# Kernel optimization log

Measured on AMD Instinct MI355X. Metric: run time of the kernel, lower is better.

Reference implementation:

```python
import jax, jax.numpy as jnp
import numpy as np

B, T, D, V, MEM = 2, 512, 512, 256, 256


def _gru(x, h0, wih, whh, bih, bhh):
    # x: [B,T,D], h0: [B,D]; torch GRU gate order: r, z, n
    def step(h, xt):
        gi = xt @ wih.T + bih            # [B,3D]
        gh = h @ whh.T + bhh             # [B,3D]
        i_r, i_z, i_n = jnp.split(gi, 3, axis=-1)
        h_r, h_z, h_n = jnp.split(gh, 3, axis=-1)
        r = jax.nn.sigmoid(i_r + h_r)
        z = jax.nn.sigmoid(i_z + h_z)
        n = jnp.tanh(i_n + r * h_n)
        h_new = (1.0 - z) * n + z * h
        return h_new, h_new
    hT, ys = jax.lax.scan(step, h0, jnp.swapaxes(x, 0, 1))
    return jnp.swapaxes(ys, 0, 1), hT


def _layernorm(x, g, b, eps=1e-5):
    m = jnp.mean(x, axis=-1, keepdims=True)
    v = jnp.mean((x - m) ** 2, axis=-1, keepdims=True)
    return (x - m) / jnp.sqrt(v + eps) * g + b


def setup_inputs() -> dict:
    key = jax.random.key(0)
    ks = jax.random.split(key, 24)
    s = 1.0 / np.sqrt(D)
    inp = {
        'x': jax.random.randint(ks[0], (B, T), 0, V, dtype=jnp.int32),
        'h_f': jnp.zeros((1, B, D), jnp.float32),
        'h_s': jnp.zeros((1, B, D), jnp.float32),
        'soma_w': jax.random.normal(ks[1], (V, D), jnp.float32),
        'fast_wih': jax.random.normal(ks[2], (3 * D, D)) * s,
        'fast_whh': jax.random.normal(ks[3], (3 * D, D)) * s,
        'fast_bih': jax.random.normal(ks[4], (3 * D,)) * s,
        'fast_bhh': jax.random.normal(ks[5], (3 * D,)) * s,
        'slow_wih': jax.random.normal(ks[6], (3 * D, D)) * s,
        'slow_whh': jax.random.normal(ks[7], (3 * D, D)) * s,
        'slow_bih': jax.random.normal(ks[8], (3 * D,)) * s,
        'slow_bhh': jax.random.normal(ks[9], (3 * D,)) * s,
        'qkv_w': jax.random.normal(ks[10], (3 * D, D)) * s,
        'qkv_b': jax.random.normal(ks[11], (3 * D,)) * s,
        'gate_w': jax.random.normal(ks[12], (D, D)) * s,
        'gate_b': jax.random.normal(ks[13], (D,)) * s,
        'gate_g': jnp.ones((D,), jnp.float32),
        'gate_bb': jnp.zeros((D,), jnp.float32),
        'mem_bank': jax.random.normal(ks[14], (MEM, D)) * 0.1,
        'hip_qw': jax.random.normal(ks[15], (D, D)) * s,
        'hip_qb': jax.random.normal(ks[16], (D,)) * s,
        'axon_w': jax.random.normal(ks[17], (D, 4 * D)) * (0.5 * s),
        'axon_b': jax.random.normal(ks[18], (D,)) * s,
        'norm_g': jnp.ones((D,), jnp.float32),
        'norm_b': jnp.zeros((D,), jnp.float32),
    }
    return inp


def reference(x, h_f, h_s, soma_w, fast_wih, fast_whh, fast_bih, fast_bhh,
              slow_wih, slow_whh, slow_bih, slow_bhh, qkv_w, qkv_b,
              gate_w, gate_b, gate_g, gate_bb, mem_bank, hip_qw, hip_qb,
              axon_w, axon_b, norm_g, norm_b):
    d = soma_w.shape[1]
    s_in = soma_w[x]  # mod[0] == 1.0
    p_f, hf1 = _gru(s_in, h_f[0], fast_wih, fast_whh, fast_bih, fast_bhh)
    p_s, hs1 = _gru(p_f, h_s[0], slow_wih, slow_whh, slow_bih, slow_bhh)
    # LinearIntentMemory: naive cumulative outer-product linear attention
    qkv = p_s @ qkv_w.T + qkv_b
    q, k, v = jnp.split(qkv, 3, axis=-1)
    q = jax.nn.elu(q) + 1.0
    k = jax.nn.elu(k) + 1.0
    kv_cum = jnp.cumsum(jnp.einsum('bti,btj->btij', k, v), axis=1)  # [B,T,D,D]
    num = jnp.einsum('bti,btij->btj', q, kv_cum)
    den = jnp.einsum('bti,bti->bt', q, jnp.cumsum(k, axis=1))[..., None] + 1e-6
    l_mem = num / den
    # intent gate: Linear -> LayerNorm -> Tanh
    intent = jnp.tanh(_layernorm(p_s @ gate_w.T + gate_b, gate_g, gate_bb))
    # hippocampus: softmax attention over memory bank
    qh = p_s @ hip_qw.T + hip_qb
    attn = qh @ mem_bank.T / jnp.sqrt(jnp.float32(d))
    episodes = jax.nn.softmax(attn, axis=-1) @ mem_bank
    combined = jnp.concatenate([p_f, intent, l_mem, episodes], axis=-1)
    thought = _layernorm(jnp.tanh(combined @ axon_w.T + axon_b), norm_g, norm_b)
    sw = soma_w / jnp.maximum(jnp.linalg.norm(soma_w, axis=-1, keepdims=True), 1e-12)
    logits = (thought @ sw.T) * 16.0
    return (logits, thought, hf1[None], hs1[None])
```

## Files before the change

### kernel.cpp

```cpp
#include <hip/hip_runtime.h>
#include <cstddef>

#define F_ELUQK 1
#define F_CAUSAL 2
#define F_DIV 4
#define F_NN 8
#define F_SCALE 16
#define FLAG_STRIDE 32
#define L_WGS 64
#define UNITS 8

enum : int {
  OFF_QH = 0,
  OFF_GI = 524288,
  OFF_COMB = OFF_GI + 1572864,
  OFF_PS = OFF_COMB + 2097152,
  OFF_QKV = OFF_PS + 524288,
  OFF_SCORES = OFF_QKV + 1572864,
  OFF_DEN = OFF_SCORES + 524288,
  OFF_TMP = OFF_DEN + 1024,
  OFF_ATTN = OFF_TMP + 524288,
  OFF_SW = OFF_ATTN + 262144,
  OFF_RING = OFF_SW + 131072,
  OFF_HSB = OFF_RING + 4096,
  OFF_FLAGS = OFF_HSB + 2048
};

__global__ __launch_bounds__(256) void gemm(
    const float* __restrict__ A, int lda, const float* __restrict__ B, int ldb,
    float* __restrict__ C, int ldc, int coff, int K,
    const float* __restrict__ bias, const float* __restrict__ den,
    float scale, int flags, int bBatch, const int* __restrict__ xidx) {
  __shared__ float As[16 * 65];
  __shared__ float Bs[16 * 65];
  int tid = threadIdx.x;
  int n0 = blockIdx.x * 64, m0 = blockIdx.y * 64;
  int rowoff = (m0 >> 9) * bBatch;
  int tx = tid & 15, ty = tid >> 4;

  if ((flags & F_CAUSAL) && n0 > ((m0 & 511) + 63)) {
    #pragma unroll
    for (int i = 0; i < 4; ++i)
      #pragma unroll
      for (int j = 0; j < 4; ++j)
        C[(size_t)(m0 + ty * 4 + i) * ldc + coff + n0 + tx * 4 + j] = 0.f;
    return;
  }

  float acc[4][4] = {};
  for (int k0 = 0; k0 < K; k0 += 16) {
    {
      int rr = tid >> 2, c4 = (tid & 3) << 2;
      int arow = m0 + rr;
      const float* ap = xidx ? (A + (size_t)xidx[arow] * 512 + (k0 + c4))
                             : (A + (size_t)arow * lda + (k0 + c4));
      float4 av = *(const float4*)ap;
      As[(c4 + 0) * 65 + rr] = av.x;
      As[(c4 + 1) * 65 + rr] = av.y;
      As[(c4 + 2) * 65 + rr] = av.z;
      As[(c4 + 3) * 65 + rr] = av.w;
    }
    if (!(flags & F_NN)) {
      int rr = tid >> 2, c4 = (tid & 3) << 2;
      const float* bp = B + (size_t)(n0 + rr + rowoff) * ldb + (k0 + c4);
      float4 bv = *(const float4*)bp;
      Bs[(c4 + 0) * 65 + rr] = bv.x; Bs[(c4 + 1) * 65 + rr] = bv.y;
      Bs[(c4 + 2) * 65 + rr] = bv.z; Bs[(c4 + 3) * 65 + rr] = bv.w;
    } else {
      int kk = tid >> 4, n4 = (tid & 15) << 2;
      const float* bp = B + (size_t)(k0 + kk + rowoff) * ldb + (n0 + n4);
      float4 bv = *(const float4*)bp;
      Bs[kk * 65 + n4 + 0] = bv.x; Bs[kk * 65 + n4 + 1] = bv.y;
      Bs[kk * 65 + n4 + 2] = bv.z; Bs[kk * 65 + n4 + 3] = bv.w;
    }
    __syncthreads();
    #pragma unroll
    for (int k = 0; k < 16; ++k) {
      float av[4], bv[4];
      #pragma unroll
      for (int i = 0; i < 4; ++i) av[i] = As[k * 65 + ty * 4 + i];
      #pragma unroll
      for (int j = 0; j < 4; ++j) bv[j] = Bs[k * 65 + tx * 4 + j];
      #pragma unroll
      for (int i = 0; i < 4; ++i)
        #pragma unroll
        for (int j = 0; j < 4; ++j)
          acc[i][j] = fmaf(av[i], bv[j], acc[i][j]);
    }
    __syncthreads();
  }
  #pragma unroll
  for (int i = 0; i < 4; ++i) {
    int m = m0 + ty * 4 + i;
    float dv = (flags & F_DIV) ? (1.0f / (den[m] + 1e-6f)) : 1.0f;
    #pragma unroll
    for (int j = 0; j < 4; ++j) {
      int n = n0 + tx * 4 + j;
      float v = acc[i][j];
      if (bias) v += bias[n];
      if (flags & F_ELUQK) { if (n < 1024) v = (v > 0.f) ? (v + 1.f) : __expf(v); }
      if (flags & F_CAUSAL) { if (n > (m & 511)) v = 0.f; }
      if (flags & F_SCALE) v *= scale;
      if (flags & F_DIV) v *= dv;
      C[(size_t)m * ldc + coff + n] = v;
    }
  }
}

__global__ __launch_bounds__(256) void gemm3(
    const float* __restrict__ A,
    const float* __restrict__ qkvw, const float* __restrict__ qkvb,
    const float* __restrict__ gatew, const float* __restrict__ gateb,
    const float* __restrict__ hipw, const float* __restrict__ hipb,
    float* __restrict__ QKV, float* __restrict__ TMP, float* __restrict__ QH) {
  __shared__ float As[16 * 65];
  __shared__ float Bs[16 * 65];
  int tid = threadIdx.x;
  int n0 = blockIdx.x * 64, m0 = blockIdx.y * 64;
  const float* B; const float* bias; float* C; int ldc, base;
  if (n0 < 1536) { B = qkvw; bias = qkvb; C = QKV; ldc = 1536; base = 0; }
  else if (n0 < 2048) { B = gatew; bias = gateb; C = TMP; ldc = 512; base = 1536; }
  else { B = hipw; bias = hipb; C = QH; ldc = 512; base = 2048; }
  int tx = tid & 15, ty = tid >> 4;
  float acc[4][4] = {};
  for (int k0 = 0; k0 < 512; k0 += 16) {
    {
      int rr = tid >> 2, c4 = (tid & 3) << 2;
      const float* ap = A + (size_t)(m0 + rr) * 512 + (k0 + c4);
      float4 av = *(const float4*)ap;
      As[(c4 + 0) * 65 + rr] = av.x; As[(c4 + 1) * 65 + rr] = av.y;
      As[(c4 + 2) * 65 + rr] = av.z; As[(c4 + 3) * 65 + rr] = av.w;
    }
    {
      int rr = tid >> 2, c4 = (tid & 3) << 2;
      const float* bp = B + (size_t)(n0 - base + rr) * 512 + (k0 + c4);
      float4 bv = *(const float4*)bp;
      Bs[(c4 + 0) * 65 + rr] = bv.x; Bs[(c4 + 1) * 65 + rr] = bv.y;
      Bs[(c4 + 2) * 65 + rr] = bv.z; Bs[(c4 + 3) * 65 + rr] = bv.w;
    }
    __syncthreads();
    #pragma unroll
    for (int k = 0; k < 16; ++k) {
      float av[4], bv[4];
      #pragma unroll
      for (int i = 0; i < 4; ++i) av[i] = As[k * 65 + ty * 4 + i];
      #pragma unroll
      for (int j = 0; j < 4; ++j) bv[j] = Bs[k * 65 + tx * 4 + j];
      #pragma unroll
      for (int i = 0; i < 4; ++i)
        #pragma unroll
        for (int j = 0; j < 4; ++j)
          acc[i][j] = fmaf(av[i], bv[j], acc[i][j]);
    }
    __syncthreads();
  }
  #pragma unroll
  for (int i = 0; i < 4; ++i) {
    int m = m0 + ty * 4 + i;
    #pragma unroll
    for (int j = 0; j < 4; ++j) {
      int n = n0 + tx * 4 + j;
      float v = acc[i][j] + bias[n - base];
      if (n < 1024) v = (v > 0.f) ? (v + 1.f) : __expf(v);
      C[(size_t)m * ldc + (n - base)] = v;
    }
  }
}

__device__ __forceinline__ void post_flag(unsigned* flags, int w, unsigned v) {
  __hip_atomic_store(flags + (size_t)w * FLAG_STRIDE, v, __ATOMIC_RELAXED,
                     __HIP_MEMORY_SCOPE_AGENT);
}
__device__ __forceinline__ void poll64(const unsigned* flags, unsigned tgt, int lane) {
  const unsigned* p = flags + (size_t)lane * FLAG_STRIDE;
  while (__hip_atomic_load(p, __ATOMIC_RELAXED, __HIP_MEMORY_SCOPE_AGENT) < tgt)
    __builtin_amdgcn_s_sleep(1);
}

__global__ __launch_bounds__(256, 1) void gru2_kernel(
    const float* __restrict__ gi,
    const float* __restrict__ fwhh, const float* __restrict__ fbhh,
    const float* __restrict__ h0f,
    const float* __restrict__ swih, const float* __restrict__ sbih,
    const float* __restrict__ swhh, const float* __restrict__ sbhh,
    const float* __restrict__ h0s,
    float* __restrict__ pf_out,
    float* __restrict__ ps_out,
    float* __restrict__ hfT, float* __restrict__ hsT,
    float* __restrict__ ring,
    float* __restrict__ hsbuf,
    unsigned* __restrict__ flagsA, unsigned* __restrict__ flagsB) {
  __shared__ __attribute__((aligned(16))) float hl[1024];
  __shared__ __attribute__((aligned(16))) float hfs[1024];
  __shared__ float P[48];
  __shared__ float Q[48];
  __shared__ float bl[24];
  __shared__ float bi[24];
  int tid = threadIdx.x, wg = blockIdx.x;
  bool L1 = wg < L_WGS;
  int j0 = (wg & (L_WGS - 1)) * UNITS;
  int part = tid & 7, r = tid >> 3;
  int g = r >> 3, u = r & 7;
  int wave = tid >> 6, lane = tid & 63;
  const float* whh = L1 ? fwhh : swhh;
  const float* bhh = L1 ? fbhh : sbhh;

  float4 wh[16], wi[16];
  if (r < 24) {
    const float* wp = whh + (size_t)(g * 512 + j0 + u) * 512 + part * 4;
    #pragma unroll
    for (int i = 0; i < 16; ++i) wh[i] = *(const float4*)(wp + i * 32);
    if (!L1) {
      const float* wp2 = swih + (size_t)(g * 512 + j0 + u) * 512 + part * 4;
      #pragma unroll
      for (int i = 0; i < 16; ++i) wi[i] = *(const float4*)(wp2 + i * 32);
    }
  }
  if (tid < 24) {
    bl[tid] = bhh[(tid >> 3) * 512 + j0 + (tid & 7)];
    if (!L1) bi[tid] = sbih[(tid >> 3) * 512 + j0 + (tid & 7)];
  }

  unsigned long long* hlq = (unsigned long long*)hl;
  unsigned long long* hfq = (unsigned long long*)hfs;
  const float4* h4 = (const float4*)hl;
  const float4* f4v = (const float4*)hfs;

  if (L1) {
    for (int t = 0; t < 512; ++t) {
      float i_r = 0.f, i_z = 0.f, i_n = 0.f;
      if (tid < 16) {
        int b = tid >> 3, jl = tid & 7;
        const float* girow = gi + (size_t)(b * 512 + t) * 1536 + j0 + jl;
        i_r = girow[0]; i_z = girow[512]; i_n = girow[1024];
      }
      if (wave == 0) {
        if (t > 0) poll64(flagsA, (unsigned)t, lane);
        unsigned long long v[8];
        if (t == 0) {
          const unsigned long long* s8 = (const unsigned long long*)h0f;
          #pragma unroll
          for (int k = 0; k < 8; ++k) v[k] = s8[k * 64 + lane];
        } else {
          const unsigned long long* s8 =
              (const unsigned long long*)(ring + ((t - 1) & 3) * 1024);
          #pragma unroll
          for (int k = 0; k < 8; ++k)
            v[k] = __hip_atomic_load(s8 + k * 64 + lane, __ATOMIC_RELAXED,
                                     __HIP_MEMORY_SCOPE_AGENT);
        }
        #pragma unroll
        for (int k = 0; k < 8; ++k) hlq[k * 64 + lane] = v[k];
      } else if (wave == 1) {
        if (t >= 4) poll64(flagsB, (unsigned)(t - 3), lane);
      }
      __syncthreads();
      if (r < 24) {
        float a0 = 0.f, a1 = 0.f;
        #pragma unroll
        for (int i = 0; i < 16; ++i) {
          float4 w = wh[i];
          float4 x0 = h4[i * 8 + part];
          float4 x1 = h4[128 + i * 8 + part];
          a0 += w.x * x0.x + w.y * x0.y + w.z * x0.z + w.w * x0.w;
          a1 += w.x * x1.x + w.y * x1.y + w.z * x1.z + w.w * x1.w;
        }
        a0 += __shfl_xor(a0, 1); a0 += __shfl_xor(a0, 2); a0 += __shfl_xor(a0, 4);
        a1 += __shfl_xor(a1, 1); a1 += __shfl_xor(a1, 2); a1 += __shfl_xor(a1, 4);
        if (part == 0) { P[r] = a0; P[24 + r] = a1; }
      }
      __syncthreads();
      if (tid < 16) {
        int b = tid >> 3, u2 = tid & 7, j = j0 + u2;
        float gh_r = P[b * 24 + u2] + bl[u2];
        float gh_z = P[b * 24 + 8 + u2] + bl[8 + u2];
        float gh_n = P[b * 24 + 16 + u2] + bl[16 + u2];
        float hold = hl[b * 512 + j];
        float rg = 1.0f / (1.0f + __expf(-(i_r + gh_r)));
        float zg = 1.0f / (1.0f + __expf(-(i_z + gh_z)));
        float ng = tanhf(i_n + rg * gh_n);
        float hnew = (1.0f - zg) * ng + zg * hold;
        __hip_atomic_store(ring + (size_t)(t & 3) * 1024 + b * 512 + j, hnew,
                           __ATOMIC_RELAXED, __HIP_MEMORY_SCOPE_AGENT);
        pf_out[(size_t)(b * 512 + t) * 2048 + j] = hnew;
        if (t == 511) hfT[b * 512 + j] = hnew;
      }
      __syncthreads();
      if (tid == 0) post_flag(flagsA, wg, (unsigned)(t + 1));
    }
  } else {
    for (int t2 = 0; t2 < 512; ++t2) {
      if (wave == 0) {
        poll64(flagsA, (unsigned)(t2 + 1), lane);
        const unsigned long long* f8 =
            (const unsigned long long*)(ring + (t2 & 3) * 1024);
        unsigned long long v[8];
        #pragma unroll
        for (int k = 0; k < 8; ++k)
          v[k] = __hip_atomic_load(f8 + k * 64 + lane, __ATOMIC_RELAXED,
                                   __HIP_MEMORY_SCOPE_AGENT);
        #pragma unroll
        for (int k = 0; k < 8; ++k) hfq[k * 64 + lane] = v[k];
      } else if (wave == 1) {
        unsigned long long v[8];
        if (t2 == 0) {
          const unsigned long long* s8 = (const unsigned long long*)h0s;
          #pragma unroll
          for (int k = 0; k < 8; ++k) v[k] = s8[k * 64 + lane];
        } else {
          poll64(flagsB, (unsigned)t2, lane);
          const unsigned long long* s8 =
              (const unsigned long long*)(hsbuf + ((t2 - 1) & 1) * 1024);
          #pragma unroll
          for (int k = 0; k < 8; ++k)
            v[k] = __hip_atomic_load(s8 + k * 64 + lane, __ATOMIC_RELAXED,
                                     __HIP_MEMORY_SCOPE_AGENT);
        }
        #pragma unroll
        for (int k = 0; k < 8; ++k) hlq[k * 64 + lane] = v[k];
      }
      __syncthreads();
      if (r < 24) {
        float a0 = 0.f, a1 = 0.f, c0 = 0.f, c1 = 0.f;
        #pragma unroll
        for (int i = 0; i < 16; ++i) {
          float4 w = wh[i];
          float4 x0 = h4[i * 8 + part];
          float4 x1 = h4[128 + i * 8 + part];
          a0 += w.x * x0.x + w.y * x0.y + w.z * x0.z + w.w * x0.w;
          a1 += w.x * x1.x + w.y * x1.y + w.z * x1.z + w.w * x1.w;
          float4 v = wi[i];
          float4 y0 = f4v[i * 8 + part];
          float4 y1 = f4v[128 + i * 8 + part];
          c0 += v.x * y0.x + v.y * y0.y + v.z * y0.z + v.w * y0.w;
          c1 += v.x * y1.x + v.y * y1.y + v.z * y1.z + v.w * y1.w;
        }
        a0 += __shfl_xor(a0, 1); a0 += __shfl_xor(a0, 2); a0 += __shfl_xor(a0, 4);
        a1 += __shfl_xor(a1, 1); a1 += __shfl_xor(a1, 2); a1 += __shfl_xor(a1, 4);
        c0 += __shfl_xor(c0, 1); c0 += __shfl_xor(c0, 2); c0 += __shfl_xor(c0, 4);
        c1 += __shfl_xor(c1, 1); c1 += __shfl_xor(c1, 2); c1 += __shfl_xor(c1, 4);
        if (part == 0) { P[r] = a0; P[24 + r] = a1; Q[r] = c0; Q[24 + r] = c1; }
      }
      __syncthreads();
      if (tid < 16) {
        int b = tid >> 3, u2 = tid & 7, j = j0 + u2;
        float i_r = Q[b * 24 + u2] + bi[u2];
        float i_z = Q[b * 24 + 8 + u2] + bi[8 + u2];
        float i_n = Q[b * 24 + 16 + u2] + bi[16 + u2];
        float gh_r = P[b * 24 + u2] + bl[u2];
        float gh_z = P[b * 24 + 8 + u2] + bl[8 + u2];
        float gh_n = P[b * 24 + 16 + u2] + bl[16 + u2];
        float hold = hl[b * 512 + j];
        float rg = 1.0f / (1.0f + __expf(-(i_r + gh_r)));
        float zg = 1.0f / (1.0f + __expf(-(i_z + gh_z)));
        float ng = tanhf(i_n + rg * gh_n);
        float hnew = (1.0f - zg) * ng + zg * hold;
        __hip_atomic_store(hsbuf + (size_t)(t2 & 1) * 1024 + b * 512 + j, hnew,
                           __ATOMIC_RELAXED, __HIP_MEMORY_SCOPE_AGENT);
        ps_out[(size_t)(b * 512 + t2) * 512 + j] = hnew;
        if (t2 == 511) hsT[b * 512 + j] = hnew;
      }
      __syncthreads();
      if (tid == 0) post_flag(flagsB, wg - L_WGS, (unsigned)(t2 + 1));
    }
  }
}

__global__ __launch_bounds__(256) void rowsum_kernel(const float* __restrict__ S,
                                                     float* __restrict__ den) {
  int m = blockIdx.x, tid = threadIdx.x;
  float s = S[(size_t)m * 512 + tid] + S[(size_t)m * 512 + 256 + tid];
  #pragma unroll
  for (int off = 32; off > 0; off >>= 1) s += __shfl_down(s, off);
  __shared__ float r4[4];
  if ((tid & 63) == 0) r4[tid >> 6] = s;
  __syncthreads();
  if (tid == 0) den[m] = r4[0] + r4[1] + r4[2] + r4[3];
}

__global__ __launch_bounds__(256) void softmax_kernel(float* __restrict__ a) {
  int m = blockIdx.x, tid = threadIdx.x;
  float v = a[(size_t)m * 256 + tid];
  float mx = v;
  #pragma unroll
  for (int off = 32; off > 0; off >>= 1) mx = fmaxf(mx, __shfl_down(mx, off));
  __shared__ float r4[4];
  __shared__ float s4[4];
  if ((tid & 63) == 0) r4[tid >> 6] = mx;
  __syncthreads();
  mx = fmaxf(fmaxf(r4[0], r4[1]), fmaxf(r4[2], r4[3]));
  float e = __expf(v - mx);
  float s = e;
  #pragma unroll
  for (int off = 32; off > 0; off >>= 1) s += __shfl_down(s, off);
  if ((tid & 63) == 0) s4[tid >> 6] = s;
  __syncthreads();
  s = s4[0] + s4[1] + s4[2] + s4[3];
  a[(size_t)m * 256 + tid] = e / s;
}

__global__ __launch_bounds__(256) void ln_kernel(
    const float* __restrict__ src, float* __restrict__ dst, int ldd, int dcoff,
    const float* __restrict__ gv, const float* __restrict__ bv, int tanhFirst) {
  int m = blockIdx.x, tid = threadIdx.x;
  float x0 = src[(size_t)m * 512 + tid];
  float x1 = src[(size_t)m * 512 + 256 + tid];
  if (tanhFirst) { x0 = tanhf(x0); x1 = tanhf(x1); }
  float s = x0 + x1, ss = x0 * x0 + x1 * x1;
  #pragma unroll
  for (int off = 32; off > 0; off >>= 1) { s += __shfl_down(s, off); ss += __shfl_down(ss, off); }
  __shared__ float rs[4], rss[4];
  if ((tid & 63) == 0) { rs[tid >> 6] = s; rss[tid >> 6] = ss; }
  __syncthreads();
  float st = rs[0] + rs[1] + rs[2] + rs[3];
  float sst = rss[0] + rss[1] + rss[2] + rss[3];
  float mean = st * (1.0f / 512.0f);
  float var = sst * (1.0f / 512.0f) - mean * mean;
  float inv = rsqrtf(var + 1e-5f);
  float y0 = (x0 - mean) * inv * gv[tid] + bv[tid];
  float y1 = (x1 - mean) * inv * gv[256 + tid] + bv[256 + tid];
  if (!tanhFirst) { y0 = tanhf(y0); y1 = tanhf(y1); }
  dst[(size_t)m * ldd + dcoff + tid] = y0;
  dst[(size_t)m * ldd + dcoff + 256 + tid] = y1;
}

__global__ __launch_bounds__(256) void swnorm_kernel(const float* __restrict__ soma,
                                                     float* __restrict__ sw) {
  int r = blockIdx.x, tid = threadIdx.x;
  float x0 = soma[(size_t)r * 512 + tid];
  float x1 = soma[(size_t)r * 512 + 256 + tid];
  float ss = x0 * x0 + x1 * x1;
  #pragma unroll
  for (int off = 32; off > 0; off >>= 1) ss += __shfl_down(ss, off);
  __shared__ float r4[4];
  if ((tid & 63) == 0) r4[tid >> 6] = ss;
  __syncthreads();
  float norm = sqrtf(r4[0] + r4[1] + r4[2] + r4[3]);
  norm = fmaxf(norm, 1e-12f);
  float inv = 1.0f / norm;
  sw[(size_t)r * 512 + tid] = x0 * inv;
  sw[(size_t)r * 512 + 256 + tid] = x1 * inv;
}

extern "C" void kernel_launch(void* const* d_in, const int* in_sizes, int n_in,
                              void* d_out, int out_size, void* d_ws, size_t ws_size,
                              hipStream_t stream) {
  (void)in_sizes; (void)n_in; (void)out_size; (void)ws_size;
  float* W = (float*)d_ws;
  float* outf = (float*)d_out;
  const int* x = (const int*)d_in[0];
  const float* soma = (const float*)d_in[3];

  hipMemsetAsync((char*)d_ws + (size_t)OFF_FLAGS * 4, 0, 16384, stream);

  gemm<<<dim3(24, 16), 256, 0, stream>>>(soma, 512, (const float*)d_in[4], 512,
      W + OFF_GI, 1536, 0, 512, (const float*)d_in[6], nullptr, 1.f, 0, 0, x);

  gru2_kernel<<<2 * L_WGS, 256, 0, stream>>>(W + OFF_GI,
      (const float*)d_in[5], (const float*)d_in[7], (const float*)d_in[1],
      (const float*)d_in[8], (const float*)d_in[10],
      (const float*)d_in[9], (const float*)d_in[11], (const float*)d_in[2],
      W + OFF_COMB, W + OFF_PS, outf + 786432, outf + 787456,
      W + OFF_RING, W + OFF_HSB,
      (unsigned*)(W + OFF_FLAGS), (unsigned*)(W + OFF_FLAGS) + L_WGS * FLAG_STRIDE);

  gemm3<<<dim3(40, 16), 256, 0, stream>>>(W + OFF_PS,
      (const float*)d_in[12], (const float*)d_in[13],
      (const float*)d_in[14], (const float*)d_in[15],
      (const float*)d_in[19], (const float*)d_in[20],
      W + OFF_QKV, W + OFF_TMP, W + OFF_QH);

  gemm<<<dim3(8, 16), 256, 0, stream>>>(W + OFF_QKV, 1536, W + OFF_QKV + 512, 1536,
      W + OFF_SCORES, 512, 0, 512, nullptr, nullptr, 1.f, F_CAUSAL, 512, nullptr);

  rowsum_kernel<<<1024, 256, 0, stream>>>(W + OFF_SCORES, W + OFF_DEN);

  gemm<<<dim3(8, 16), 256, 0, stream>>>(W + OFF_SCORES, 512, W + OFF_QKV + 1024, 1536,
      W + OFF_COMB, 2048, 1024, 512, nullptr, W + OFF_DEN, 1.f, F_NN | F_DIV, 512, nullptr);

  ln_kernel<<<1024, 256, 0, stream>>>(W + OFF_TMP, W + OFF_COMB, 2048, 512,
      (const float*)d_in[16], (const float*)d_in[17], 0);

  gemm<<<dim3(4, 16), 256, 0, stream>>>(W + OFF_QH, 512, (const float*)d_in[18], 512,
      W + OFF_ATTN, 256, 0, 512, nullptr, nullptr, 0.04419417382415922f, F_SCALE, 0, nullptr);
  softmax_kernel<<<1024, 256, 0, stream>>>(W + OFF_ATTN);
  gemm<<<dim3(8, 16), 256, 0, stream>>>(W + OFF_ATTN, 256, (const float*)d_in[18], 512,
      W + OFF_COMB, 2048, 1536, 256, nullptr, nullptr, 1.f, F_NN, 0, nullptr);

  gemm<<<dim3(8, 16), 256, 0, stream>>>(W + OFF_COMB, 2048, (const float*)d_in[21], 2048,
      W + OFF_TMP, 512, 0, 2048, (const float*)d_in[22], nullptr, 1.f, 0, 0, nullptr);
  ln_kernel<<<1024, 256, 0, stream>>>(W + OFF_TMP, outf + 262144, 512, 0,
      (const float*)d_in[23], (const float*)d_in[24], 1);

  swnorm_kernel<<<256, 256, 0, stream>>>(soma, W + OFF_SW);
  gemm<<<dim3(4, 16), 256, 0, stream>>>(outf + 262144, 512, W + OFF_SW, 512,
      outf, 256, 0, 512, nullptr, nullptr, 16.f, F_SCALE, 0, nullptr);
}
```

Baseline: 2.082 ms.

## Fuse rowsum into scores GEMM, split-K axon GEMM, column-scale logits, lighter GRU flags

After: 2.171 ms. 4.3% more time.

```diff
diff --git a/kernel.cpp b/kernel.cpp
--- a/kernel.cpp
+++ b/kernel.cpp
@@ -6,6 +6,7 @@
 #define F_DIV 4
 #define F_NN 8
 #define F_SCALE 16
+#define F_ROWSUM 32
 #define FLAG_STRIDE 32
 #define L_WGS 64
 #define UNITS 8
@@ -20,8 +21,8 @@
   OFF_DEN = OFF_SCORES + 524288,
   OFF_TMP = OFF_DEN + 1024,
   OFF_ATTN = OFF_TMP + 524288,
-  OFF_SW = OFF_ATTN + 262144,
-  OFF_RING = OFF_SW + 131072,
+  OFF_SWN = OFF_ATTN + 262144,
+  OFF_RING = OFF_SWN + 256,
   OFF_HSB = OFF_RING + 4096,
   OFF_FLAGS = OFF_HSB + 2048
 };
@@ -30,11 +31,14 @@
     const float* __restrict__ A, int lda, const float* __restrict__ B, int ldb,
     float* __restrict__ C, int ldc, int coff, int K,
     const float* __restrict__ bias, const float* __restrict__ den,
-    float scale, int flags, int bBatch, const int* __restrict__ xidx) {
+    const float* __restrict__ cscale, float* __restrict__ rsum,
+    float scale, int flags, int bBatch, const int* __restrict__ xidx,
+    float* __restrict__ Cz, int kzoff) {
   __shared__ float As[16 * 65];
   __shared__ float Bs[16 * 65];
   int tid = threadIdx.x;
   int n0 = blockIdx.x * 64, m0 = blockIdx.y * 64;
+  if (blockIdx.z) { A += kzoff; B += kzoff; C = Cz; bias = nullptr; }
   int rowoff = (m0 >> 9) * bBatch;
   int tx = tid & 15, ty = tid >> 4;
 
@@ -89,6 +93,7 @@
     }
     __syncthreads();
   }
+  float rs[4] = {0.f, 0.f, 0.f, 0.f};
   #pragma unroll
   for (int i = 0; i < 4; ++i) {
     int m = m0 + ty * 4 + i;
@@ -101,8 +106,19 @@
       if (flags & F_ELUQK) { if (n < 1024) v = (v > 0.f) ? (v + 1.f) : __expf(v); }
       if (flags & F_CAUSAL) { if (n > (m & 511)) v = 0.f; }
       if (flags & F_SCALE) v *= scale;
+      if (cscale) v *= cscale[coff + n];
       if (flags & F_DIV) v *= dv;
       C[(size_t)m * ldc + coff + n] = v;
+      if (flags & F_ROWSUM) rs[i] += v;
+    }
+  }
+  if (flags & F_ROWSUM) {
+    #pragma unroll
+    for (int i = 0; i < 4; ++i) {
+      float s = rs[i];
+      s += __shfl_xor(s, 1); s += __shfl_xor(s, 2);
+      s += __shfl_xor(s, 4); s += __shfl_xor(s, 8);
+      if (tx == 0) atomicAdd(rsum + (m0 + ty * 4 + i), s);
     }
   }
 }
@@ -285,8 +301,10 @@
         pf_out[(size_t)(b * 512 + t) * 2048 + j] = hnew;
         if (t == 511) hfT[b * 512 + j] = hnew;
       }
-      __syncthreads();
-      if (tid == 0) post_flag(flagsA, wg, (unsigned)(t + 1));
+      if (tid == 0) {
+        __builtin_amdgcn_s_waitcnt(0);
+        post_flag(flagsA, wg, (unsigned)(t + 1));
+      }
     }
   } else {
     for (int t2 = 0; t2 < 512; ++t2) {
@@ -360,22 +378,12 @@
         ps_out[(size_t)(b * 512 + t2) * 512 + j] = hnew;
         if (t2 == 511) hsT[b * 512 + j] = hnew;
       }
-      __syncthreads();
-      if (tid == 0) post_flag(flagsB, wg - L_WGS, (unsigned)(t2 + 1));
-    }
-  }
-}
-
-__global__ __launch_bounds__(256) void rowsum_kernel(const float* __restrict__ S,
-                                                     float* __restrict__ den) {
-  int m = blockIdx.x, tid = threadIdx.x;
-  float s = S[(size_t)m * 512 + tid] + S[(size_t)m * 512 + 256 + tid];
-  #pragma unroll
-  for (int off = 32; off > 0; off >>= 1) s += __shfl_down(s, off);
-  __shared__ float r4[4];
-  if ((tid & 63) == 0) r4[tid >> 6] = s;
-  __syncthreads();
-  if (tid == 0) den[m] = r4[0] + r4[1] + r4[2] + r4[3];
+      if (tid == 0) {
+        __builtin_amdgcn_s_waitcnt(0);
+        post_flag(flagsB, wg - L_WGS, (unsigned)(t2 + 1));
+      }
+    }
+  }
 }
 
 __global__ __launch_bounds__(256) void softmax_kernel(float* __restrict__ a) {
@@ -400,11 +408,13 @@
 }
 
 __global__ __launch_bounds__(256) void ln_kernel(
-    const float* __restrict__ src, float* __restrict__ dst, int ldd, int dcoff,
+    const float* __restrict__ src, const float* __restrict__ src2,
+    float* __restrict__ dst, int ldd, int dcoff,
     const float* __restrict__ gv, const float* __restrict__ bv, int tanhFirst) {
   int m = blockIdx.x, tid = threadIdx.x;
   float x0 = src[(size_t)m * 512 + tid];
   float x1 = src[(size_t)m * 512 + 256 + tid];
+  if (src2) { x0 += src2[(size_t)m * 512 + tid]; x1 += src2[(size_t)m * 512 + 256 + tid]; }
   if (tanhFirst) { x0 = tanhf(x0); x1 = tanhf(x1); }
   float s = x0 + x1, ss = x0 * x0 + x1 * x1;
   #pragma unroll
@@ -424,8 +434,8 @@
   dst[(size_t)m * ldd + dcoff + 256 + tid] = y1;
 }
 
-__global__ __launch_bounds__(256) void swnorm_kernel(const float* __restrict__ soma,
-                                                     float* __restrict__ sw) {
+__global__ __launch_bounds__(256) void swinv_kernel(const float* __restrict__ soma,
+                                                    float* __restrict__ swn) {
   int r = blockIdx.x, tid = threadIdx.x;
   float x0 = soma[(size_t)r * 512 + tid];
   float x1 = soma[(size_t)r * 512 + 256 + tid];
@@ -435,11 +445,10 @@
   __shared__ float r4[4];
   if ((tid & 63) == 0) r4[tid >> 6] = ss;
   __syncthreads();
-  float norm = sqrtf(r4[0] + r4[1] + r4[2] + r4[3]);
-  norm = fmaxf(norm, 1e-12f);
-  float inv = 1.0f / norm;
-  sw[(size_t)r * 512 + tid] = x0 * inv;
-  sw[(size_t)r * 512 + 256 + tid] = x1 * inv;
+  if (tid == 0) {
+    float norm = fmaxf(sqrtf(r4[0] + r4[1] + r4[2] + r4[3]), 1e-12f);
+    swn[r] = 16.0f / norm;
+  }
 }
 
 extern "C" void kernel_launch(void* const* d_in, const int* in_sizes, int n_in,
@@ -452,9 +461,11 @@
   const float* soma = (const float*)d_in[3];
 
   hipMemsetAsync((char*)d_ws + (size_t)OFF_FLAGS * 4, 0, 16384, stream);
+  hipMemsetAsync((char*)d_ws + (size_t)OFF_DEN * 4, 0, 4096, stream);
 
   gemm<<<dim3(24, 16), 256, 0, stream>>>(soma, 512, (const float*)d_in[4], 512,
-      W + OFF_GI, 1536, 0, 512, (const float*)d_in[6], nullptr, 1.f, 0, 0, x);
+      W + OFF_GI, 1536, 0, 512, (const float*)d_in[6], nullptr, nullptr, nullptr,
+      1.f, 0, 0, x, nullptr, 0);
 
   gru2_kernel<<<2 * L_WGS, 256, 0, stream>>>(W + OFF_GI,
       (const float*)d_in[5], (const float*)d_in[7], (const float*)d_in[1],
@@ -471,28 +482,33 @@
       W + OFF_QKV, W + OFF_TMP, W + OFF_QH);
 
   gemm<<<dim3(8, 16), 256, 0, stream>>>(W + OFF_QKV, 1536, W + OFF_QKV + 512, 1536,
-      W + OFF_SCORES, 512, 0, 512, nullptr, nullptr, 1.f, F_CAUSAL, 512, nullptr);
-
-  rowsum_kernel<<<1024, 256, 0, stream>>>(W + OFF_SCORES, W + OFF_DEN);
+      W + OFF_SCORES, 512, 0, 512, nullptr, nullptr, nullptr, W + OFF_DEN,
+      1.f, F_CAUSAL | F_ROWSUM, 512, nullptr, nullptr, 0);
 
   gemm<<<dim3(8, 16), 256, 0, stream>>>(W + OFF_SCORES, 512, W + OFF_QKV + 1024, 1536,
-      W + OFF_COMB, 2048, 1024, 512, nullptr, W + OFF_DEN, 1.f, F_NN | F_DIV, 512, nullptr);
-
-  ln_kernel<<<1024, 256, 0, stream>>>(W + OFF_TMP, W + OFF_COMB, 2048, 512,
+      W + OFF_COMB, 2048, 1024, 512, nullptr, W + OFF_DEN, nullptr, nullptr,
+      1.f, F_NN | F_DIV, 512, nullptr, nullptr, 0);
+
+  ln_kernel<<<1024, 256, 0, stream>>>(W + OFF_TMP, nullptr, W + OFF_COMB, 2048, 512,
       (const float*)d_in[16], (const float*)d_in[17], 0);
 
   gemm<<<dim3(4, 16), 256, 0, stream>>>(W + OFF_QH, 512, (const float*)d_in[18], 512,
-      W + OFF_ATTN, 256, 0, 512, nullptr, nullptr, 0.04419417382415922f, F_SCALE, 0, nullptr);
+      W + OFF_ATTN, 256, 0, 512, nullptr, nullptr, nullptr, nullptr,
+      0.04419417382415922f, F_SCALE, 0, nullptr, nullptr, 0);
   softmax_kernel<<<1024, 256, 0, stream>>>(W + OFF_ATTN);
   gemm<<<dim3(8, 16), 256, 0, stream>>>(W + OFF_ATTN, 256, (const float*)d_in[18], 512,
-      W + OFF_COMB, 2048, 1536, 256, nullptr, nullptr, 1.f, F_NN, 0, nullptr);
-
-  gemm<<<dim3(8, 16), 256, 0, stream>>>(W + OFF_COMB, 2048, (const float*)d_in[21], 2048,
-      W + OFF_TMP, 512, 0, 2048, (const float*)d_in[22], nullptr, 1.f, 0, 0, nullptr);
-  ln_kernel<<<1024, 256, 0, stream>>>(W + OFF_TMP, outf + 262144, 512, 0,
+      W + OFF_COMB, 2048, 1536, 256, nullptr, nullptr, nullptr, nullptr,
+      1.f, F_NN, 0, nullptr, nullptr, 0);
+
+  gemm<<<dim3(8, 16, 2), 256, 0, stream>>>(W + OFF_COMB, 2048, (const float*)d_in[21], 2048,
+      W + OFF_TMP, 512, 0, 1024, (const float*)d_in[22], nullptr, nullptr, nullptr,
+      1.f, 0, 0, nullptr, W + OFF_QH, 1024);
+
+  ln_kernel<<<1024, 256, 0, stream>>>(W + OFF_TMP, W + OFF_QH, outf + 262144, 512, 0,
       (const float*)d_in[23], (const float*)d_in[24], 1);
 
-  swnorm_kernel<<<256, 256, 0, stream>>>(soma, W + OFF_SW);
-  gemm<<<dim3(4, 16), 256, 0, stream>>>(outf + 262144, 512, W + OFF_SW, 512,
-      outf, 256, 0, 512, nullptr, nullptr, 16.f, F_SCALE, 0, nullptr);
-}
+  swinv_kernel<<<256, 256, 0, stream>>>(soma, W + OFF_SWN);
+  gemm<<<dim3(4, 16), 256, 0, stream>>>(outf + 262144, 512, soma, 512,
+      outf, 256, 0, 512, nullptr, nullptr, W + OFF_SWN, nullptr,
+      1.f, 0, 0, nullptr, nullptr, 0);
+}
```
